# Kernel optimization log

Measured on AMD Instinct MI355X. Metric: run time of the kernel, lower is better.

## Reference

```python
import jax, jax.numpy as jnp
import numpy as np

T = 4096        # sequence length
D = 128         # input feature dim
TRACE = 64      # trace_size
CONTEXT = 64    # context_size
HID = 64        # internal dense width (hardcoded 64 in module)
OUT = 128       # output_size
LN_EPS = 1e-6   # flax LayerNorm default epsilon


def setup_inputs() -> dict:
    key = jax.random.key(0)
    ks = jax.random.split(key, 12)

    def dense(k, fi, fo):
        return (jax.random.normal(k, (fi, fo), jnp.float32) / np.sqrt(fi).astype(np.float32))

    inp = {}
    inp["x"] = jax.random.normal(ks[0], (T, D), jnp.float32)
    inp["state"] = jnp.zeros((1, TRACE, CONTEXT), jnp.complex64)
    inp["start"] = jax.random.uniform(ks[1], (T,)) < 0.01  # sparse episode resets
    # deterministic FFM decay / frequency params (init_deterministic)
    inp["a"] = jnp.linspace(1e-6, 0.5, TRACE).astype(jnp.float32)
    inp["b"] = (2.0 * jnp.pi / jnp.linspace(1.0, 1000.0, CONTEXT)).astype(jnp.float32)
    inp["W1"] = dense(ks[2], D, HID);               inp["b1"] = jnp.zeros((HID,), jnp.float32)
    inp["W2"] = dense(ks[3], HID, 2 * TRACE);       inp["b2"] = jnp.zeros((2 * TRACE,), jnp.float32)
    inp["Wgi"] = dense(ks[4], 2 * TRACE, TRACE);    inp["bgi"] = jnp.zeros((TRACE,), jnp.float32)
    inp["Wp"] = dense(ks[5], 2 * TRACE, TRACE);     inp["bp"] = jnp.zeros((TRACE,), jnp.float32)
    inp["Wz"] = dense(ks[6], 2 * TRACE * CONTEXT, HID); inp["bz"] = jnp.zeros((HID,), jnp.float32)
    inp["Wgo"] = dense(ks[7], 2 * TRACE, HID);      inp["bgo"] = jnp.zeros((HID,), jnp.float32)
    inp["Ws"] = dense(ks[8], 2 * TRACE, HID);       inp["bs"] = jnp.zeros((HID,), jnp.float32)
    inp["W3"] = dense(ks[9], HID, HID);             inp["b3"] = jnp.zeros((HID,), jnp.float32)
    inp["W4"] = dense(ks[10], HID, OUT);            inp["b4"] = jnp.zeros((OUT,), jnp.float32)
    return inp


def _ffm_scan(scan_in, state0, start, a, b):
    # scan_in: (T, TRACE, CONTEXT) float, state0: (1, TRACE, CONTEXT) complex64
    t = scan_in.shape[0]
    timestep = jnp.ones((t + 1, 1, 1), dtype=jnp.int32)
    start_f = jnp.concatenate(
        [jnp.zeros((1, 1, 1), dtype=bool), start.reshape(t, 1, 1)], axis=0)
    xs = jnp.concatenate([state0, scan_in.astype(jnp.complex64)], axis=0)

    neg_a = -jnp.abs(a).reshape(1, TRACE, 1)
    b_r = b.reshape(1, 1, CONTEXT)
    ab = neg_a + 1j * b_r  # (1, TRACE, CONTEXT) complex

    def gamma(j):
        # j: (N,1,1) int -> (N, TRACE, CONTEXT) complex decay
        return jnp.exp(ab * j.astype(jnp.float32))

    def combine(carry, incoming):
        prev_start, s, i = carry
        st, xx, j = incoming
        keep = jnp.logical_not(st)
        s = s * keep
        j = j * keep.astype(j.dtype)
        new_s = s * gamma(j) + xx
        return (jnp.logical_or(st, prev_start), new_s, j + i)

    _, new_state, _ = jax.lax.associative_scan(
        combine, (start_f, xs, timestep), axis=0)
    return new_state[1:]  # (T, TRACE, CONTEXT) complex64


def _layernorm(x):
    mu = jnp.mean(x, axis=-1, keepdims=True)
    var = jnp.var(x, axis=-1, keepdims=True)
    return (x - mu) * jax.lax.rsqrt(var + LN_EPS)


def _forward(x, state, start, a, b, W1, b1, W2, b2, Wgi, bgi, Wp, bp,
             Wz, bz, Wgo, bgo, Ws, bs, W3, b3, W4, b4):
    h = jax.nn.relu(x @ W1 + b1)                 # (T, 64)
    h2 = h @ W2 + b2                             # (T, 2*TRACE)
    gate_in = jax.nn.sigmoid(h2 @ Wgi + bgi)     # (T, TRACE)
    pre = jax.nn.sigmoid(h2 @ Wp + bp)           # (T, TRACE)
    gated = pre * gate_in                        # (T, TRACE)
    scan_in = jnp.broadcast_to(gated[:, :, None], (gated.shape[0], TRACE, CONTEXT))
    state_seq = _ffm_scan(scan_in, state, start, a, b)  # (T, TRACE, CONTEXT) c64
    z_in = jnp.concatenate([jnp.real(state_seq), jnp.imag(state_seq)],
                           axis=-1).reshape(state_seq.shape[0], -1)
    z = z_in @ Wz + bz                           # (T, 64)
    gate_out = jax.nn.sigmoid(h2 @ Wgo + bgo)    # (T, 64)
    skip = h2 @ Ws + bs                          # (T, 64)
    out = _layernorm(z * gate_out) + skip * (1.0 - gate_out)
    out = jax.nn.relu(out @ W3 + b3)
    out = out @ W4 + b4                          # (T, OUT)
    return out, state_seq[-1:]


def reference(x, state, start, a, b, W1, b1, W2, b2, Wgi, bgi, Wp, bp,
              Wz, bz, Wgo, bgo, Ws, bs, W3, b3, W4, b4):
    return _forward(x, state, start, a, b, W1, b1, W2, b2, Wgi, bgi, Wp, bp,
                    Wz, bz, Wgo, bgo, Ws, bs, W3, b3, W4, b4)
```

## Files before the change

### kernel.cpp

```cpp
#include <hip/hip_runtime.h>
#include <math.h>

#define T_LEN 4096
#define D_IN 128
#define HID 64
#define KDIM 4096
#define K2   8192

#define OFF_GATED 0u
#define OFF_GO    262144u
#define OFF_SKIP  524288u
#define OFF_PART  786432u
#define OFF_FLAGS 2883584u
#define OFF_CHS   2887680u
#define OFF_WZT   2887744u
#define OFF_STBF  3149888u

typedef __attribute__((ext_vector_type(8))) short short8v;
typedef __attribute__((ext_vector_type(4))) float float4v;

__device__ __forceinline__ float sigm(float x){ return 1.f/(1.f+expf(-x)); }
__device__ __forceinline__ unsigned short f2bf(float x){
    unsigned int u = __float_as_uint(x);
    return (unsigned short)((u + 0x7FFFu + ((u >> 16) & 1u)) >> 16);
}

__global__ __launch_bounds__(512) void k_prep(
    const unsigned char* __restrict__ su8, const int* __restrict__ si32,
    int* __restrict__ flags, int* __restrict__ chunkStart,
    const float* __restrict__ Wz, unsigned short* __restrict__ wzt,
    const float* __restrict__ x,
    const float* __restrict__ W1, const float* __restrict__ b1,
    const float* __restrict__ W2, const float* __restrict__ b2,
    const float* __restrict__ Wgi, const float* __restrict__ bgi,
    const float* __restrict__ Wp,  const float* __restrict__ bp,
    const float* __restrict__ Wgo, const float* __restrict__ bgo,
    const float* __restrict__ Wsk, const float* __restrict__ bsk,
    float* __restrict__ gated, float* __restrict__ go, float* __restrict__ sk)
{
    const int bx = blockIdx.x;
    const int tid = threadIdx.x;

    if (bx == 0) {
        __shared__ int cnt;
        if (tid == 0) cnt = 0;
        __syncthreads();
        int local = 0;
        for (int i = tid; i < 4096; i += 512)
            if (i & 3) local += su8[i];
        if (local) atomicAdd(&cnt, local);
        __syncthreads();
        if (cnt > 0) {
            for (int i = tid; i < 4096; i += 512) flags[i] = su8[i] ? 1 : 0;
        } else {
            for (int i = tid; i < 4096; i += 512) flags[i] = si32[i] ? 1 : 0;
        }
        __syncthreads();
        if (tid < 64) {
            int any = 0;
#pragma unroll 8
            for (int j = 0; j < 64; ++j) any |= flags[tid * 64 + j];
            chunkStart[tid] = any;
        }
        return;
    }
    if (bx <= 64) {
        int idx = ((bx - 1) * 512 + tid) * 16;
        int j = idx >> 13, k0 = idx & 8191;
#pragma unroll
        for (int e = 0; e < 16; ++e) {
            int k = k0 + e;
            wzt[(size_t)j * K2 + k] = f2bf(Wz[(size_t)k * 64 + j]);
        }
        return;
    }

    __shared__ float xs[8][128];
    __shared__ float hs[8][64];
    __shared__ float h2s[8][128];
    __shared__ float tmp[8][4][64];
    const int t0 = (bx - 65) * 8;

    if (tid < 256) {
        int r = tid >> 5, kq = (tid & 31) << 2;
        *(float4*)&xs[r][kq] = *(const float4*)&x[(size_t)(t0 + r) * D_IN + kq];
    }

    const int j1 = tid >> 3, ks1 = tid & 7;
    float wr1[16];
#pragma unroll
    for (int kk = 0; kk < 16; ++kk) wr1[kk] = W1[(size_t)(ks1 * 16 + kk) * HID + j1];
    const float bias1 = b1[j1];
    __syncthreads();
#pragma unroll
    for (int r = 0; r < 8; ++r) {
        float p = 0.f;
#pragma unroll
        for (int kq = 0; kq < 4; ++kq) {
            float4 xv = *(const float4*)&xs[r][ks1 * 16 + kq * 4];
            p += xv.x * wr1[kq*4] + xv.y * wr1[kq*4+1] + xv.z * wr1[kq*4+2] + xv.w * wr1[kq*4+3];
        }
        p += __shfl_xor(p, 1, 64); p += __shfl_xor(p, 2, 64); p += __shfl_xor(p, 4, 64);
        if (ks1 == 0) hs[r][j1] = fmaxf(p + bias1, 0.f);
    }

    const int j2 = tid >> 2, ks2 = tid & 3;
    float wr2[16];
#pragma unroll
    for (int kk = 0; kk < 16; ++kk) wr2[kk] = W2[(size_t)(ks2 * 16 + kk) * 128 + j2];
    const float bias2 = b2[j2];
    __syncthreads();
#pragma unroll
    for (int r = 0; r < 8; ++r) {
        float p = 0.f;
#pragma unroll
        for (int kq = 0; kq < 4; ++kq) {
            float4 hv = *(const float4*)&hs[r][ks2 * 16 + kq * 4];
            p += hv.x * wr2[kq*4] + hv.y * wr2[kq*4+1] + hv.z * wr2[kq*4+2] + hv.w * wr2[kq*4+3];
        }
        p += __shfl_xor(p, 1, 64); p += __shfl_xor(p, 2, 64);
        if (ks2 == 0) h2s[r][j2] = p + bias2;
    }

    const int mat = tid >> 7, jj = (tid & 127) >> 1, kh = tid & 1;
    const float* Wm = (mat == 0) ? Wgi : (mat == 1) ? Wp : (mat == 2) ? Wgo : Wsk;
    float wgr[64];
#pragma unroll
    for (int kk = 0; kk < 64; ++kk) wgr[kk] = Wm[(size_t)(kh * 64 + kk) * 64 + jj];
    __syncthreads();
#pragma unroll
    for (int r = 0; r < 8; ++r) {
        float p = 0.f;
#pragma unroll
        for (int kq = 0; kq < 16; ++kq) {
            float4 hv = *(const float4*)&h2s[r][kh * 64 + kq * 4];
            p += hv.x * wgr[kq*4] + hv.y * wgr[kq*4+1] + hv.z * wgr[kq*4+2] + hv.w * wgr[kq*4+3];
        }
        p += __shfl_xor(p, 1, 64);
        if (kh == 0) tmp[r][mat][jj] = p;
    }
    __syncthreads();

    {
        int r = tid >> 6, j = tid & 63;
        int t = t0 + r;
        float gi = sigm(tmp[r][0][j] + bgi[j]);
        float pr = sigm(tmp[r][1][j] + bp[j]);
        float g  = sigm(tmp[r][2][j] + bgo[j]);
        float s  = tmp[r][3][j] + bsk[j];
        gated[t * 64 + j] = gi * pr;
        go[t * 64 + j]    = g;
        sk[t * 64 + j]    = s;
    }
}

__global__ __launch_bounds__(512) void k_scanA(
    const float* __restrict__ gated, const int* __restrict__ flags,
    const float* __restrict__ a, const float* __restrict__ b,
    float2* __restrict__ carryB)
{
    const int p = threadIdx.x >> 6, c = threadIdx.x & 63;
    const int pair = blockIdx.x * 8 + p;
    const int ch = pair & 63, m = pair >> 6;
    const int t0 = ch * 64;
    __shared__ float gb[8][64];
    __shared__ int fb[8][64];
    gb[p][c] = gated[(size_t)(t0 + c) * 64 + m];
    fb[p][c] = flags[t0 + c];
    __syncthreads();

    const double ea = exp(-fabs((double)a[m]));
    const double bb = (double)b[c];
    const double lre = ea * cos(bb), lim = ea * sin(bb);
    double sre = 0.0, sim = 0.0;
#pragma unroll 8
    for (int j = 0; j < 64; ++j) {
        double g = (double)gb[p][j];
        if (fb[p][j]) { sre = g; sim = 0.0; }
        else {
            double nr = fma(sre, lre, fma(-sim, lim, g));
            double ni = fma(sre, lim, sim * lre);
            sre = nr; sim = ni;
        }
    }
    carryB[(size_t)ch * KDIM + m * 64 + c] = make_float2((float)sre, (float)sim);
}

__global__ __launch_bounds__(64) void k_scanC(
    const float2* __restrict__ carryB, const int* __restrict__ chunkStart,
    const float* __restrict__ a, const float* __restrict__ b,
    const float* __restrict__ st0,
    float2* __restrict__ cinArr)
{
    const int m = blockIdx.x, c = threadIdx.x;
    __shared__ int chsS[64];
    chsS[c] = chunkStart[c];

    float2 Bv[64];
#pragma unroll
    for (int ch = 0; ch < 64; ++ch)
        Bv[ch] = carryB[(size_t)ch * KDIM + m * 64 + c];
    __syncthreads();

    const double ea64 = exp(-64.0 * fabs((double)a[m]));
    const double bb = (double)b[c];
    const double l64re = ea64 * cos(64.0 * bb), l64im = ea64 * sin(64.0 * bb);
    double cre = (double)st0[(m * 64 + c) * 2];
    double cim = (double)st0[(m * 64 + c) * 2 + 1];
#pragma unroll
    for (int ch = 0; ch < 64; ++ch) {
        cinArr[(size_t)ch * KDIM + m * 64 + c] = make_float2((float)cre, (float)cim);
        if (chsS[ch]) { cre = (double)Bv[ch].x; cim = (double)Bv[ch].y; }
        else {
            double nr = fma(cre, l64re, fma(-cim, l64im, (double)Bv[ch].x));
            double ni = fma(cre, l64im, fma(cim, l64re, (double)Bv[ch].y));
            cre = nr; cim = ni;
        }
    }
}

__global__ __launch_bounds__(256) void k_scanB(
    const float* __restrict__ gated, const int* __restrict__ flags,
    const float* __restrict__ a, const float* __restrict__ b,
    const float2* __restrict__ cinArr,
    unsigned short* __restrict__ stbf,
    float* __restrict__ out)
{
    const int tid = threadIdx.x;
    const int ml = tid >> 6, c = tid & 63;
    const int ch = blockIdx.x & 63, mg = blockIdx.x >> 6;
    const int m = mg * 4 + ml;
    const int t0 = ch * 64;
    __shared__ unsigned short st[64][512];
    __shared__ float gb[4][64];
    __shared__ int fb[64];
    gb[ml][c] = gated[(size_t)(t0 + c) * 64 + m];
    if (ml == 0) fb[c] = flags[t0 + c];
    __syncthreads();

    const double ea = exp(-fabs((double)a[m]));
    const double bb = (double)b[c];
    const double lre = ea * cos(bb), lim = ea * sin(bb);
    float2 cin = cinArr[(size_t)ch * KDIM + m * 64 + c];
    double sre = (double)cin.x, sim = (double)cin.y;
#pragma unroll 4
    for (int j = 0; j < 64; ++j) {
        double g = (double)gb[ml][j];
        if (fb[j]) { sre = g; sim = 0.0; }
        else {
            double nr = fma(sre, lre, fma(-sim, lim, g));
            double ni = fma(sre, lim, sim * lre);
            sre = nr; sim = ni;
        }
        st[j][ml * 128 + c]      = f2bf((float)sre);
        st[j][ml * 128 + 64 + c] = f2bf((float)sim);
    }
    __syncthreads();

#pragma unroll
    for (int it = 0; it < 16; ++it) {
        int idx = it * 256 + tid;
        int row = idx >> 6, colB = (idx & 63) * 16;
        *(uint4*)((char*)(stbf + (size_t)(t0 + row) * K2 + mg * 512) + colB) =
            *(const uint4*)((const char*)st + row * 1024 + colB);
    }
    if (ch == 63) {
        out[524288 + m * 64 + c]        = (float)sre;
        out[524288 + 4096 + m * 64 + c] = (float)sim;
    }
}

__global__ __launch_bounds__(256) void k_zgemm(
    const unsigned short* __restrict__ stbf,
    const unsigned short* __restrict__ wzt,
    float* __restrict__ part)
{
    __shared__ char smem[65536];
    const int tid = threadIdx.x;
    const int w = tid >> 6, l = tid & 63;
    const int mb = blockIdx.x >> 3, kb = blockIdx.x & 7;
    const int kbase = kb * 1024;

    float4v acc[4];
#pragma unroll
    for (int i = 0; i < 4; ++i) acc[i] = (float4v){0.f, 0.f, 0.f, 0.f};

#define ZSTAGE(s, d)                                                                              \
    _Pragma("unroll")                                                                             \
    for (int it = 0; it < 4; ++it) {                                                              \
        int ci = it * 256 + tid;                                                                  \
        int r = ci >> 4, pc = ci & 15;                                                            \
        int gc = pc ^ (r & 7);                                                                    \
        const unsigned short* gpA = stbf + (size_t)(mb * 64 + r) * K2 + kbase + (s) * 128 + gc * 8;\
        const unsigned short* gpB = wzt + (size_t)r * K2 + kbase + (s) * 128 + gc * 8;            \
        __builtin_amdgcn_global_load_lds(                                                         \
            (const __attribute__((address_space(1))) void*)gpA,                                   \
            (__attribute__((address_space(3))) void*)(smem + (d) * 32768 + ci * 16), 16, 0, 0);   \
        __builtin_amdgcn_global_load_lds(                                                         \
            (const __attribute__((address_space(1))) void*)gpB,                                   \
            (__attribute__((address_space(3))) void*)(smem + (d) * 32768 + 16384 + ci * 16), 16, 0, 0); \
    }

    ZSTAGE(0, 0);
    __syncthreads();
    const int row_l = w * 16 + (l & 15);
    const int swz = (l & 7) << 4;
    const int ksub = (l >> 4) * 16;
#pragma unroll
    for (int s = 0; s < 8; ++s) {
        const int cur = s & 1;
        if (s < 7) { ZSTAGE(s + 1, cur ^ 1); }
        const char* bufA = smem + cur * 32768;
        const char* bufB = bufA + 16384;
#pragma unroll
        for (int k32 = 0; k32 < 4; ++k32) {
            int kbyte = k32 * 64 + ksub;
            short8v af = *(const short8v*)(bufA + row_l * 256 + (kbyte ^ swz));
#pragma unroll
            for (int nt = 0; nt < 4; ++nt) {
                int row_b = nt * 16 + (l & 15);
                short8v bf = *(const short8v*)(bufB + row_b * 256 + (kbyte ^ swz));
                acc[nt] = __builtin_amdgcn_mfma_f32_16x16x32_bf16(af, bf, acc[nt], 0, 0, 0);
            }
        }
        __syncthreads();
    }
#undef ZSTAGE

    float* pp = part + (size_t)kb * 262144;
    const int trow = mb * 64 + w * 16 + (l >> 4) * 4;
    const int jcol = l & 15;
#pragma unroll
    for (int nt = 0; nt < 4; ++nt)
#pragma unroll
        for (int r = 0; r < 4; ++r)
            pp[(size_t)(trow + r) * 64 + nt * 16 + jcol] = acc[nt][r];
}

__device__ __forceinline__ float wsum(float v) {
#pragma unroll
    for (int o = 32; o; o >>= 1) v += __shfl_xor(v, o, 64);
    return v;
}

__global__ __launch_bounds__(256) void k_epi(
    const float* __restrict__ part, const float* __restrict__ bz,
    const float* __restrict__ go, const float* __restrict__ sk,
    const float* __restrict__ W3, const float* __restrict__ b3,
    const float* __restrict__ W4, const float* __restrict__ b4,
    float* __restrict__ out)
{
    __shared__ float ob[4][64], hb[4][64];
    const int w = threadIdx.x >> 6, j = threadIdx.x & 63;
    const int t = blockIdx.x * 4 + w;
    float z = bz[j];
#pragma unroll
    for (int p = 0; p < 8; ++p) z += part[(size_t)p * 262144 + t * 64 + j];
    float g = go[t * 64 + j];
    float y = z * g;
    float mu = wsum(y) * 0.015625f;
    float d = y - mu;
    float var = wsum(d * d) * 0.015625f;
    float o = d * (1.f / sqrtf(var + 1e-6f)) + sk[t * 64 + j] * (1.f - g);
    ob[w][j] = o;
    __syncthreads();
    float acc = b3[j];
#pragma unroll 8
    for (int k = 0; k < 64; ++k) acc += ob[w][k] * W3[k * 64 + j];
    hb[w][j] = fmaxf(acc, 0.f);
    __syncthreads();
    float o1 = b4[j], o2 = b4[j + 64];
#pragma unroll 8
    for (int k = 0; k < 64; ++k) { float hv = hb[w][k]; o1 += hv * W4[k * 128 + j]; o2 += hv * W4[k * 128 + j + 64]; }
    out[(size_t)t * 128 + j] = o1;
    out[(size_t)t * 128 + j + 64] = o2;
}

extern "C" void kernel_launch(void* const* d_in, const int* in_sizes, int n_in,
                              void* d_out, int out_size, void* d_ws, size_t ws_size,
                              hipStream_t stream)
{
    const float* x   = (const float*)d_in[0];
    const float* st0 = (const float*)d_in[1];
    const void*  start = d_in[2];
    const float* a  = (const float*)d_in[3];
    const float* b  = (const float*)d_in[4];
    const float* W1 = (const float*)d_in[5];  const float* b1 = (const float*)d_in[6];
    const float* W2 = (const float*)d_in[7];  const float* b2 = (const float*)d_in[8];
    const float* Wgi= (const float*)d_in[9];  const float* bgi= (const float*)d_in[10];
    const float* Wp = (const float*)d_in[11]; const float* bp = (const float*)d_in[12];
    const float* Wz = (const float*)d_in[13]; const float* bz = (const float*)d_in[14];
    const float* Wgo= (const float*)d_in[15]; const float* bgo= (const float*)d_in[16];
    const float* Wsk= (const float*)d_in[17]; const float* bsk= (const float*)d_in[18];
    const float* W3 = (const float*)d_in[19]; const float* b3 = (const float*)d_in[20];
    const float* W4 = (const float*)d_in[21]; const float* b4 = (const float*)d_in[22];

    float* ws    = (float*)d_ws;
    float* out   = (float*)d_out;
    float* gated = ws + OFF_GATED;
    float* go    = ws + OFF_GO;
    float* sk    = ws + OFF_SKIP;
    float* part  = ws + OFF_PART;
    int*   flags = (int*)(ws + OFF_FLAGS);
    int*   chs   = (int*)(ws + OFF_CHS);
    unsigned short* wzt  = (unsigned short*)(ws + OFF_WZT);
    unsigned short* stbf = (unsigned short*)(ws + OFF_STBF);

    float2* carryB = (float2*)(part);
    float2* cinArr = (float2*)(part + 524288);

    hipLaunchKernelGGL(k_prep, dim3(577), dim3(512), 0, stream,
                       (const unsigned char*)start, (const int*)start, flags, chs,
                       Wz, wzt, x, W1, b1, W2, b2, Wgi, bgi, Wp, bp,
                       Wgo, bgo, Wsk, bsk, gated, go, sk);
    hipLaunchKernelGGL(k_scanA, dim3(512), dim3(512), 0, stream,
                       gated, flags, a, b, carryB);
    hipLaunchKernelGGL(k_scanC, dim3(64), dim3(64), 0, stream,
                       carryB, chs, a, b, st0, cinArr);
    hipLaunchKernelGGL(k_scanB, dim3(1024), dim3(256), 0, stream,
                       gated, flags, a, b, cinArr, stbf, out);
    hipLaunchKernelGGL(k_zgemm, dim3(512), dim3(256), 0, stream, stbf, wzt, part);
    hipLaunchKernelGGL(k_epi, dim3(1024), dim3(256), 0, stream,
                       part, bz, go, sk, W3, b3, W4, b4, out);
}
```

Measured before the change: 95.62 us.

## Fuse scan state production into the Wz GEMM, keeping bf16 state in LDS

The scan kernel now multiplies its bf16 state tile, held in a swizzled LDS buffer, directly against Wz fragments loaded into registers. This removes the global write and re-read of the large state matrix and one kernel launch. The cost is that each of the 16 trace groups writes its own split-K partial, so the epilogue sums 16 partials instead of 8, which doubles partial-buffer traffic. The workspace offsets are moved so the larger partial buffer fits.

```diff
diff --git a/kernel.cpp b/kernel.cpp
--- a/kernel.cpp
+++ b/kernel.cpp
@@ -11,10 +11,10 @@
 #define OFF_GO    262144u
 #define OFF_SKIP  524288u
 #define OFF_PART  786432u
-#define OFF_FLAGS 2883584u
-#define OFF_CHS   2887680u
-#define OFF_WZT   2887744u
-#define OFF_STBF  3149888u
+#define OFF_FLAGS 4980736u
+#define OFF_CHS   4984832u
+#define OFF_WZT   4984896u
+#define OFF_SCR   5247040u
 
 typedef __attribute__((ext_vector_type(8))) short short8v;
 typedef __attribute__((ext_vector_type(4))) float float4v;
@@ -219,11 +219,12 @@
     }
 }
 
-__global__ __launch_bounds__(256) void k_scanB(
+__global__ __launch_bounds__(256) void k_scanBZ(
     const float* __restrict__ gated, const int* __restrict__ flags,
     const float* __restrict__ a, const float* __restrict__ b,
     const float2* __restrict__ cinArr,
-    unsigned short* __restrict__ stbf,
+    const unsigned short* __restrict__ wzt,
+    float* __restrict__ part,
     float* __restrict__ out)
 {
     const int tid = threadIdx.x;
@@ -231,7 +232,7 @@
     const int ch = blockIdx.x & 63, mg = blockIdx.x >> 6;
     const int m = mg * 4 + ml;
     const int t0 = ch * 64;
-    __shared__ unsigned short st[64][512];
+    __shared__ unsigned short st[64 * 512];
     __shared__ float gb[4][64];
     __shared__ int fb[64];
     gb[ml][c] = gated[(size_t)(t0 + c) * 64 + m];
@@ -243,6 +244,7 @@
     const double lre = ea * cos(bb), lim = ea * sin(bb);
     float2 cin = cinArr[(size_t)ch * KDIM + m * 64 + c];
     double sre = (double)cin.x, sim = (double)cin.y;
+    const int e0 = ml * 128 + c, e1 = ml * 128 + 64 + c;
 #pragma unroll 4
     for (int j = 0; j < 64; ++j) {
         double g = (double)gb[ml][j];
@@ -252,89 +254,47 @@
             double ni = fma(sre, lim, sim * lre);
             sre = nr; sim = ni;
         }
-        st[j][ml * 128 + c]      = f2bf((float)sre);
-        st[j][ml * 128 + 64 + c] = f2bf((float)sim);
-    }
-    __syncthreads();
-
-#pragma unroll
-    for (int it = 0; it < 16; ++it) {
-        int idx = it * 256 + tid;
-        int row = idx >> 6, colB = (idx & 63) * 16;
-        *(uint4*)((char*)(stbf + (size_t)(t0 + row) * K2 + mg * 512) + colB) =
-            *(const uint4*)((const char*)st + row * 1024 + colB);
+        const int sx = (j & 7) << 3;
+        st[j * 512 + (e0 ^ sx)] = f2bf((float)sre);
+        st[j * 512 + (e1 ^ sx)] = f2bf((float)sim);
     }
     if (ch == 63) {
         out[524288 + m * 64 + c]        = (float)sre;
         out[524288 + 4096 + m * 64 + c] = (float)sim;
     }
-}
-
-__global__ __launch_bounds__(256) void k_zgemm(
-    const unsigned short* __restrict__ stbf,
-    const unsigned short* __restrict__ wzt,
-    float* __restrict__ part)
-{
-    __shared__ char smem[65536];
-    const int tid = threadIdx.x;
-    const int w = tid >> 6, l = tid & 63;
-    const int mb = blockIdx.x >> 3, kb = blockIdx.x & 7;
-    const int kbase = kb * 1024;
+
+    const int l = c;
+    const int jrow = ml * 16 + (l & 15);
+    short8v bfr[16];
+#pragma unroll
+    for (int ks = 0; ks < 16; ++ks)
+        bfr[ks] = *(const short8v*)&wzt[(size_t)jrow * K2 + mg * 512 + (ks * 4 + (l >> 4)) * 8];
+
+    __syncthreads();
 
     float4v acc[4];
 #pragma unroll
     for (int i = 0; i < 4; ++i) acc[i] = (float4v){0.f, 0.f, 0.f, 0.f};
-
-#define ZSTAGE(s, d)                                                                              \
-    _Pragma("unroll")                                                                             \
-    for (int it = 0; it < 4; ++it) {                                                              \
-        int ci = it * 256 + tid;                                                                  \
-        int r = ci >> 4, pc = ci & 15;                                                            \
-        int gc = pc ^ (r & 7);                                                                    \
-        const unsigned short* gpA = stbf + (size_t)(mb * 64 + r) * K2 + kbase + (s) * 128 + gc * 8;\
-        const unsigned short* gpB = wzt + (size_t)r * K2 + kbase + (s) * 128 + gc * 8;            \
-        __builtin_amdgcn_global_load_lds(                                                         \
-            (const __attribute__((address_space(1))) void*)gpA,                                   \
-            (__attribute__((address_space(3))) void*)(smem + (d) * 32768 + ci * 16), 16, 0, 0);   \
-        __builtin_amdgcn_global_load_lds(                                                         \
-            (const __attribute__((address_space(1))) void*)gpB,                                   \
-            (__attribute__((address_space(3))) void*)(smem + (d) * 32768 + 16384 + ci * 16), 16, 0, 0); \
-    }
-
-    ZSTAGE(0, 0);
-    __syncthreads();
-    const int row_l = w * 16 + (l & 15);
-    const int swz = (l & 7) << 4;
-    const int ksub = (l >> 4) * 16;
-#pragma unroll
-    for (int s = 0; s < 8; ++s) {
-        const int cur = s & 1;
-        if (s < 7) { ZSTAGE(s + 1, cur ^ 1); }
-        const char* bufA = smem + cur * 32768;
-        const char* bufB = bufA + 16384;
-#pragma unroll
-        for (int k32 = 0; k32 < 4; ++k32) {
-            int kbyte = k32 * 64 + ksub;
-            short8v af = *(const short8v*)(bufA + row_l * 256 + (kbyte ^ swz));
-#pragma unroll
-            for (int nt = 0; nt < 4; ++nt) {
-                int row_b = nt * 16 + (l & 15);
-                short8v bf = *(const short8v*)(bufB + row_b * 256 + (kbyte ^ swz));
-                acc[nt] = __builtin_amdgcn_mfma_f32_16x16x32_bf16(af, bf, acc[nt], 0, 0, 0);
-            }
-        }
-        __syncthreads();
-    }
-#undef ZSTAGE
-
-    float* pp = part + (size_t)kb * 262144;
-    const int trow = mb * 64 + w * 16 + (l >> 4) * 4;
-    const int jcol = l & 15;
-#pragma unroll
-    for (int nt = 0; nt < 4; ++nt)
+#pragma unroll
+    for (int ks = 0; ks < 16; ++ks) {
+#pragma unroll
+        for (int mt = 0; mt < 4; ++mt) {
+            const int row = mt * 16 + (l & 15);
+            const int rchunk = (ks * 4 + (l >> 4)) ^ (row & 7);
+            short8v af = *(const short8v*)&st[row * 512 + rchunk * 8];
+            acc[mt] = __builtin_amdgcn_mfma_f32_16x16x32_bf16(af, bfr[ks], acc[mt], 0, 0, 0);
+        }
+    }
+
+    float* pp = part + (size_t)mg * 262144;
+    const int jcol = ml * 16 + (l & 15);
+#pragma unroll
+    for (int mt = 0; mt < 4; ++mt) {
+        const int trow = t0 + mt * 16 + (l >> 4) * 4;
 #pragma unroll
         for (int r = 0; r < 4; ++r)
-            pp[(size_t)(trow + r) * 64 + nt * 16 + jcol] = acc[nt][r];
+            pp[(size_t)(trow + r) * 64 + jcol] = acc[mt][r];
+    }
 }
 
 __device__ __forceinline__ float wsum(float v) {
@@ -355,7 +315,7 @@
     const int t = blockIdx.x * 4 + w;
     float z = bz[j];
 #pragma unroll
-    for (int p = 0; p < 8; ++p) z += part[(size_t)p * 262144 + t * 64 + j];
+    for (int p = 0; p < 16; ++p) z += part[(size_t)p * 262144 + t * 64 + j];
     float g = go[t * 64 + j];
     float y = z * g;
     float mu = wsum(y) * 0.015625f;
@@ -404,10 +364,9 @@
     int*   flags = (int*)(ws + OFF_FLAGS);
     int*   chs   = (int*)(ws + OFF_CHS);
     unsigned short* wzt  = (unsigned short*)(ws + OFF_WZT);
-    unsigned short* stbf = (unsigned short*)(ws + OFF_STBF);
-
-    float2* carryB = (float2*)(part);
-    float2* cinArr = (float2*)(part + 524288);
+
+    float2* carryB = (float2*)(ws + OFF_SCR);
+    float2* cinArr = (float2*)(ws + OFF_SCR + 524288);
 
     hipLaunchKernelGGL(k_prep, dim3(577), dim3(512), 0, stream,
                        (const unsigned char*)start, (const int*)start, flags, chs,
@@ -417,9 +376,8 @@
                        gated, flags, a, b, carryB);
     hipLaunchKernelGGL(k_scanC, dim3(64), dim3(64), 0, stream,
                        carryB, chs, a, b, st0, cinArr);
-    hipLaunchKernelGGL(k_scanB, dim3(1024), dim3(256), 0, stream,
-                       gated, flags, a, b, cinArr, stbf, out);
-    hipLaunchKernelGGL(k_zgemm, dim3(512), dim3(256), 0, stream, stbf, wzt, part);
+    hipLaunchKernelGGL(k_scanBZ, dim3(1024), dim3(256), 0, stream,
+                       gated, flags, a, b, cinArr, wzt, part, out);
     hipLaunchKernelGGL(k_epi, dim3(1024), dim3(256), 0, stream,
                        part, bz, go, sk, W3, b3, W4, b4, out);
 }
```

Result: faster. 86.17 us (-9.9%).
